# Kernel tuning notes

Hardware: AMD Instinct MI355X
Metric: run time of the kernel (lower is better)

The kernel has to match this reference:

```python
import jax, jax.numpy as jnp
import numpy as np

B, T, DQ, DV, A, F, K = 64, 1024, 1024, 512, 512, 32, 31


def setup_inputs() -> dict:
    key = jax.random.key(0)
    ks = jax.random.split(key, 8)
    query = jax.random.normal(ks[0], (B, DQ), jnp.float32)
    values = jax.random.normal(ks[1], (B, T, DV), jnp.float32)
    # decoder-step states (as produced by init_states)
    attention_cum = jnp.zeros((B, T), jnp.float32)
    attention_old = jnp.zeros((B, T), jnp.float32)
    alpha = jnp.concatenate([jnp.ones((B, 1), jnp.float32),
                             jnp.zeros((B, T - 1), jnp.float32) + 1e-7], axis=1)
    # learned parameters (Glorot-ish scaling)
    W_query = jax.random.normal(ks[2], (DQ, A), jnp.float32) / np.sqrt(DQ)
    W_inputs = jax.random.normal(ks[3], (DV, A), jnp.float32) / np.sqrt(DV)
    v_w = jax.random.normal(ks[4], (A, 1), jnp.float32) / np.sqrt(A)
    v_b = jnp.zeros((1,), jnp.float32)
    loc_kernel = jax.random.normal(ks[5], (K, 2, F), jnp.float32) / np.sqrt(K * 2)  # WIO
    W_loc = jax.random.normal(ks[6], (F, A), jnp.float32) / np.sqrt(F)
    return {"query": query, "values": values, "attention_cum": attention_cum,
            "attention_old": attention_old, "alpha": alpha,
            "W_query": W_query, "W_inputs": W_inputs, "v_w": v_w, "v_b": v_b,
            "loc_kernel": loc_kernel, "W_loc": W_loc}


def reference(query, values, attention_cum, attention_old, alpha,
              W_query, W_inputs, v_w, v_b, loc_kernel, W_loc):
    # process_values: cached projection of encoder memory  [B,T,A]
    processed_values = jnp.einsum('btd,da->bta', values, W_inputs)
    # location features: conv over stacked (old, cum) attention  [B,T,2]->[B,T,F]
    attn_cat = jnp.stack([attention_old, attention_cum], axis=2)
    conv = jax.lax.conv_general_dilated(attn_cat, loc_kernel, window_strides=(1,),
                                        padding='SAME',
                                        dimension_numbers=('NWC', 'WIO', 'NWC'))
    processed_attn = jnp.einsum('btf,fa->bta', conv, W_loc)
    # query projection  [B,1,A]
    processed_query = (query @ W_query)[:, None, :]
    # additive score  [B,T]
    score = (jnp.tanh(processed_values + processed_query + processed_attn) @ v_w)[..., 0] + v_b
    scores_norm = jax.nn.softmax(score, axis=-1)
    # forward attention recursion
    fwd_shifted = jnp.pad(alpha[:, :-1], ((0, 0), (1, 0)))
    new_alpha = (0.5 * alpha + 0.5 * fwd_shifted + 1e-8) * scores_norm
    new_alpha = new_alpha / jnp.sum(new_alpha, axis=1, keepdims=True)
    attn_weights = new_alpha
    # updated states
    new_cum = attention_cum + scores_norm
    new_old = attn_weights
    # context vector  [B,DV]
    context = jnp.einsum('bt,btd->bd', attn_weights, values)
    return (context, attn_weights, new_cum, new_old, new_alpha)
```

## Files before the change

kernel.cpp:

```cpp
#include <hip/hip_runtime.h>
#include <hip/hip_bf16.h>
#include <cstdint>
#include <cstddef>

#define B 64
#define T 1024
#define DQ 1024
#define DV 512
#define A_DIM 512
#define F_DIM 32
#define KW 31
#define M_TOT (B*T)
#define KEXT2 576
#define NCH 9

typedef __attribute__((ext_vector_type(8))) short short8;
typedef __attribute__((ext_vector_type(4))) short short4v;
typedef __attribute__((ext_vector_type(4))) float f32x4;

static __device__ __forceinline__ unsigned short f2bf(float f) {
    unsigned int u = __builtin_bit_cast(unsigned int, f);
    u += 0x7fffu + ((u >> 16) & 1u);
    return (unsigned short)(u >> 16);
}
static __device__ __forceinline__ float bf2f(unsigned short h) {
    return __builtin_bit_cast(float, (unsigned int)h << 16);
}
static __device__ __forceinline__ short8 pack8(float4 x0, float4 x1) {
    short8 pk;
    pk[0] = (short)f2bf(x0.x); pk[1] = (short)f2bf(x0.y);
    pk[2] = (short)f2bf(x0.z); pk[3] = (short)f2bf(x0.w);
    pk[4] = (short)f2bf(x1.x); pk[5] = (short)f2bf(x1.y);
    pk[6] = (short)f2bf(x1.z); pk[7] = (short)f2bf(x1.w);
    return pk;
}
static __device__ __forceinline__ float tanh_fast(float x) {
    float e = __expf(2.0f * x);
    return 1.0f - 2.0f * __builtin_amdgcn_rcpf(e + 1.0f);
}

#define LDSDMA16(gptr, lptr)                                                        \
    __builtin_amdgcn_global_load_lds(                                               \
        (const __attribute__((address_space(1))) void*)(const void*)(gptr),         \
        (__attribute__((address_space(3))) void*)(void*)(lptr), 16, 0, 0)

__global__ void prep_kernel(const float* __restrict__ values,
                            const float* __restrict__ query, const float* __restrict__ Wq,
                            const float* __restrict__ Wi, const float* __restrict__ Wl,
                            const float* __restrict__ old_, const float* __restrict__ cum_,
                            const float* __restrict__ lk,
                            unsigned short* __restrict__ vbf, float* __restrict__ pq,
                            float* __restrict__ score, unsigned short* __restrict__ Bt,
                            unsigned short* __restrict__ convb) {
    __shared__ __align__(16) char smem[16640];
    int bid = blockIdx.x, tid = threadIdx.x;
    if (bid < 4096) {
        size_t base = (size_t)bid * 8192 + (size_t)tid * 8;
        #pragma unroll
        for (int j = 0; j < 4; ++j) {
            size_t idx = base + (size_t)j * 2048;
            float4 x0 = *(const float4*)(values + idx);
            float4 x1 = *(const float4*)(values + idx + 4);
            *(short8*)(vbf + idx) = pack8(x0, x1);
        }
    } else if (bid < 4608) {
        float (*red)[64] = (float(*)[64])smem;
        int pid = bid - 4096;
        int gid = pid * 256 + tid;
        if (gid < M_TOT) score[gid] = 0.f;
        int b = pid >> 3, a0 = (pid & 7) * 64;
        int al = tid & 63, ks = tid >> 6;
        const float* qr = query + (size_t)b * DQ + ks * 256;
        const float* wc = Wq + (size_t)(ks * 256) * A_DIM + a0 + al;
        float acc = 0.f;
        #pragma unroll 8
        for (int k = 0; k < 256; ++k) acc += qr[k] * wc[(size_t)k * A_DIM];
        red[ks][al] = acc;
        __syncthreads();
        if (ks == 0)
            pq[b * A_DIM + a0 + al] = red[0][al] + red[1][al] + red[2][al] + red[3][al];
    } else if (bid < 4680) {
        float (*tile)[65] = (float(*)[65])smem;
        int tb = bid - 4608;
        if (tb < 64) {
            int k0 = (tb >> 3) * 64, a0 = (tb & 7) * 64;
            int al = tid & 63, ko = tid >> 6;
            #pragma unroll
            for (int j = 0; j < 16; ++j) {
                int kl = j * 4 + ko;
                tile[kl][al] = Wi[(size_t)(k0 + kl) * A_DIM + a0 + al];
            }
            __syncthreads();
            int kl2 = tid & 63, ao = tid >> 6;
            #pragma unroll
            for (int j = 0; j < 16; ++j) {
                int al2 = j * 4 + ao;
                Bt[(size_t)(a0 + al2) * KEXT2 + k0 + kl2] = f2bf(tile[kl2][al2]);
            }
        } else {
            int a0 = (tb - 64) * 64;
            int al = tid & 63, ko = tid >> 6;
            #pragma unroll
            for (int j = 0; j < 8; ++j) {
                int kl = j * 4 + ko;
                tile[kl][al] = Wl[(size_t)kl * A_DIM + a0 + al];
            }
            __syncthreads();
            int kl2 = tid & 31, ao = tid >> 5;
            #pragma unroll
            for (int j = 0; j < 8; ++j) {
                int al2 = j * 8 + ao;
                Bt[(size_t)(a0 + al2) * KEXT2 + DV + kl2] = f2bf(tile[kl2][al2]);
            }
            #pragma unroll
            for (int j = 0; j < 8; ++j) {
                int idx = j * 256 + tid;
                int a_l = idx >> 5, kp = idx & 31;
                Bt[(size_t)(a0 + a_l) * KEXT2 + 544 + kp] = 0;
            }
        }
    } else {
        float* sOld = (float*)smem;
        float* sCum = sOld + 94;
        float* sLK  = sCum + 94;
        int cid = bid - 4680;
        int b = cid >> 4, t0 = (cid & 15) * 64;
        int tl = tid & 63, fg = tid >> 6;
        for (int j = tid; j < 94; j += 256) {
            int tt = t0 - 15 + j;
            bool ok = (tt >= 0 && tt < T);
            sOld[j] = ok ? old_[b * T + tt] : 0.f;
            sCum[j] = ok ? cum_[b * T + tt] : 0.f;
        }
        for (int j = tid; j < KW * 2 * F_DIM; j += 256) sLK[j] = lk[j];
        __syncthreads();
        float acc[8];
        #pragma unroll
        for (int f = 0; f < 8; ++f) acc[f] = 0.f;
        for (int k = 0; k < KW; ++k) {
            float o = sOld[tl + k], c = sCum[tl + k];
            const float* lo = &sLK[(k * 2 + 0) * F_DIM + fg * 8];
            const float* lc = &sLK[(k * 2 + 1) * F_DIM + fg * 8];
            #pragma unroll
            for (int f = 0; f < 8; ++f) acc[f] += o * lo[f] + c * lc[f];
        }
        short8 pk;
        #pragma unroll
        for (int f = 0; f < 8; ++f) pk[f] = (short)f2bf(acc[f]);
        unsigned short* dst = convb + (size_t)(b * T + t0 + tl) * 64 + fg * 8;
        *(short8*)dst = pk;
        *(short8*)(dst + 32) = (short8)0;
    }
}

template<bool VBF>
__launch_bounds__(256, 3)
__global__ void gemm_score(const float* __restrict__ values,
                           const unsigned short* __restrict__ vbf,
                           const unsigned short* __restrict__ Bt,
                           const unsigned short* __restrict__ convb,
                           const float* __restrict__ pq,
                           const float* __restrict__ vw,
                           float* __restrict__ score) {
    __shared__ __align__(16) short sA[128 * 64];
    __shared__ __align__(16) short sB[128 * 64];
    __shared__ float sPQ[128];
    __shared__ float sVW[128];
    int tid = threadIdx.x;
    int x = blockIdx.x & 7, l = blockIdx.x >> 3;
    int mt = x * 64 + (l >> 2), nq = l & 3;
    int m0 = mt * 128, n0 = nq * 128;
    int b = m0 >> 10;
    if (tid < 128) { sPQ[tid] = pq[b * A_DIM + n0 + tid]; sVW[tid] = vw[n0 + tid]; }
    int w = tid >> 6, lane = tid & 63, q = lane >> 4, l15 = lane & 15;
    int wm = w & 1, wn = w >> 1;
    f32x4 acc[4][4];
    #pragma unroll
    for (int mi = 0; mi < 4; ++mi)
        #pragma unroll
        for (int ni = 0; ni < 4; ++ni) acc[mi][ni] = (f32x4)0.f;

    for (int c = 0; c < NCH; ++c) {
        __syncthreads();
        #pragma unroll
        for (int j = 0; j < 4; ++j) {
            int slot = j * 256 + tid;
            int row = slot >> 3, seg = ((slot & 7) - row) & 7;
            const unsigned short* gB = Bt + (size_t)(n0 + row) * KEXT2 + c * 64 + seg * 8;
            LDSDMA16(gB, &sB[(j * 256 + w * 64) * 8]);
        }
        if (VBF) {
            #pragma unroll
            for (int j = 0; j < 4; ++j) {
                int slot = j * 256 + tid;
                int row = slot >> 3, seg = ((slot & 7) - row) & 7;
                const unsigned short* gA = (c < 8)
                    ? vbf + (size_t)(m0 + row) * DV + c * 64 + seg * 8
                    : convb + (size_t)(m0 + row) * 64 + seg * 8;
                LDSDMA16(gA, &sA[(j * 256 + w * 64) * 8]);
            }
        } else {
            #pragma unroll
            for (int jj = 0; jj < 4; ++jj) {
                int slot = tid * 4 + jj;
                int row = slot >> 3, sl = slot & 7, seg = (sl - row) & 7;
                short8 pk;
                if (c < 8) {
                    const float* s0 = values + (size_t)(m0 + row) * DV + c * 64 + seg * 8;
                    pk = pack8(*(const float4*)s0, *(const float4*)(s0 + 4));
                } else {
                    pk = *(const short8*)(convb + (size_t)(m0 + row) * 64 + seg * 8);
                }
                *(short8*)&sA[slot * 8] = pk;
            }
        }
        __syncthreads();
        #pragma unroll
        for (int h = 0; h < 2; ++h) {
            short8 af[4], bfr[4];
            int sgl = h * 4 + q;
            #pragma unroll
            for (int mi = 0; mi < 4; ++mi) {
                int r = wm * 64 + mi * 16 + l15;
                af[mi] = *(const short8*)&sA[r * 64 + (((sgl + r) & 7) << 3)];
            }
            #pragma unroll
            for (int ni = 0; ni < 4; ++ni) {
                int r = wn * 64 + ni * 16 + l15;
                bfr[ni] = *(const short8*)&sB[r * 64 + (((sgl + r) & 7) << 3)];
            }
            #pragma unroll
            for (int mi = 0; mi < 4; ++mi)
                #pragma unroll
                for (int ni = 0; ni < 4; ++ni)
                    acc[mi][ni] = __builtin_amdgcn_mfma_f32_16x16x32_bf16(af[mi], bfr[ni], acc[mi][ni], 0, 0, 0);
        }
    }
    #pragma unroll
    for (int mi = 0; mi < 4; ++mi) {
        #pragma unroll
        for (int r = 0; r < 4; ++r) {
            float s = 0.f;
            #pragma unroll
            for (int ni = 0; ni < 4; ++ni) {
                int col = wn * 64 + ni * 16 + l15;
                float xv = acc[mi][ni][r] + sPQ[col];
                s += tanh_fast(xv) * sVW[col];
            }
            #pragma unroll
            for (int off = 1; off < 16; off <<= 1) s += __shfl_xor(s, off, 64);
            if (l15 == 0)
                atomicAdd(&score[m0 + wm * 64 + mi * 16 + q * 4 + r], s);
        }
    }
}

__global__ void softmax_fwd(const float* __restrict__ score,
                            const float* __restrict__ alpha,
                            const float* __restrict__ cum,
                            float* __restrict__ out) {
    int b = blockIdx.x, t = threadIdx.x;
    __shared__ float sred[16];
    __shared__ float sbc;
    float sc = score[b * T + t];
    int wid = t >> 6, lane = t & 63;
    float m = sc;
    #pragma unroll
    for (int off = 32; off; off >>= 1) m = fmaxf(m, __shfl_xor(m, off, 64));
    if (lane == 0) sred[wid] = m;
    __syncthreads();
    if (t == 0) { float mm = sred[0]; for (int i = 1; i < 16; ++i) mm = fmaxf(mm, sred[i]); sbc = mm; }
    __syncthreads();
    float M = sbc;
    float e = __expf(sc - M);
    float s = e;
    #pragma unroll
    for (int off = 32; off; off >>= 1) s += __shfl_xor(s, off, 64);
    __syncthreads();
    if (lane == 0) sred[wid] = s;
    __syncthreads();
    if (t == 0) { float ss = 0.f; for (int i = 0; i < 16; ++i) ss += sred[i]; sbc = ss; }
    __syncthreads();
    float sn = e / sbc;
    float a_t = alpha[b * T + t];
    float a_p = (t > 0) ? alpha[b * T + t - 1] : 0.f;
    float ua = (0.5f * (a_t + a_p) + 1e-8f) * sn;
    float u = ua;
    #pragma unroll
    for (int off = 32; off; off >>= 1) u += __shfl_xor(u, off, 64);
    __syncthreads();
    if (lane == 0) sred[wid] = u;
    __syncthreads();
    if (t == 0) { float ss = 0.f; for (int i = 0; i < 16; ++i) ss += sred[i]; sbc = ss; }
    __syncthreads();
    float wgt = ua / sbc;
    float* attnw  = out + B * DV;
    float* ncum   = attnw + B * T;
    float* nold   = ncum + B * T;
    float* nalpha = nold + B * T;
    attnw[b * T + t]  = wgt;
    ncum[b * T + t]   = cum[b * T + t] + sn;
    nold[b * T + t]   = wgt;
    nalpha[b * T + t] = wgt;
    if (t < DV) out[b * DV + t] = 0.f;
}

__global__ void context_kernel(const float* __restrict__ values,
                               const unsigned short* __restrict__ vbf,
                               int use_bf, float* __restrict__ out) {
    __shared__ float red[4][256];
    const float* attnw = out + B * DV;
    int b = blockIdx.x >> 3, tq = (blockIdx.x >> 1) & 3, dh = blockIdx.x & 1;
    int sub = threadIdx.x >> 6, dg = threadIdx.x & 63;
    int t0 = tq * 256 + sub * 64;
    int d0 = dh * 256 + dg * 4;
    float acc[4];
    #pragma unroll
    for (int f = 0; f < 4; ++f) acc[f] = 0.f;
    if (use_bf) {
        for (int tt = 0; tt < 64; ++tt) {
            int t = t0 + tt;
            float wgt = attnw[b * T + t];
            short4v v = *(const short4v*)(vbf + (size_t)(b * T + t) * DV + d0);
            #pragma unroll
            for (int f = 0; f < 4; ++f) acc[f] += wgt * bf2f((unsigned short)v[f]);
        }
    } else {
        for (int tt = 0; tt < 64; ++tt) {
            int t = t0 + tt;
            float wgt = attnw[b * T + t];
            float4 xv = *(const float4*)(values + (size_t)(b * T + t) * DV + d0);
            acc[0] += wgt * xv.x; acc[1] += wgt * xv.y;
            acc[2] += wgt * xv.z; acc[3] += wgt * xv.w;
        }
    }
    #pragma unroll
    for (int f = 0; f < 4; ++f) red[sub][dg * 4 + f] = acc[f];
    __syncthreads();
    if (sub == 0) {
        #pragma unroll
        for (int f = 0; f < 4; ++f) {
            int di = dg * 4 + f;
            float s = red[0][di] + red[1][di] + red[2][di] + red[3][di];
            atomicAdd(&out[b * DV + dh * 256 + di], s);
        }
    }
}

extern "C" void kernel_launch(void* const* d_in, const int* in_sizes, int n_in,
                              void* d_out, int out_size, void* d_ws, size_t ws_size,
                              hipStream_t stream) {
    const float* query  = (const float*)d_in[0];
    const float* values = (const float*)d_in[1];
    const float* cum    = (const float*)d_in[2];
    const float* old_   = (const float*)d_in[3];
    const float* alpha  = (const float*)d_in[4];
    const float* Wq     = (const float*)d_in[5];
    const float* Wi     = (const float*)d_in[6];
    const float* vw     = (const float*)d_in[7];
    const float* lk     = (const float*)d_in[9];
    const float* Wl     = (const float*)d_in[10];
    float* out = (float*)d_out;
    char* ws = (char*)d_ws;
    float* ws_pq            = (float*)(ws);
    float* ws_score         = (float*)(ws + 131072);
    unsigned short* ws_Bt   = (unsigned short*)(ws + 393216);
    unsigned short* ws_conv = (unsigned short*)(ws + 1048576);
    unsigned short* ws_vbf  = (unsigned short*)(ws + 16777216);
    const bool big = ws_size >= (size_t)88080384;

    if (big) {
        prep_kernel<<<5704, 256, 0, stream>>>(values, query, Wq, Wi, Wl, old_, cum, lk,
                                              ws_vbf, ws_pq, ws_score, ws_Bt, ws_conv);
        gemm_score<true><<<2048, 256, 0, stream>>>(values, ws_vbf, ws_Bt, ws_conv, ws_pq, vw, ws_score);
    } else {
        prep_kernel<<<1608, 256, 0, stream>>>(values, query, Wq, Wi, Wl, old_, cum, lk,
                                              ws_vbf, ws_pq, ws_score, ws_Bt, ws_conv);
        gemm_score<false><<<2048, 256, 0, stream>>>(values, ws_vbf, ws_Bt, ws_conv, ws_pq, vw, ws_score);
    }
    softmax_fwd<<<64, 1024, 0, stream>>>(ws_score, alpha, cum, out);
    context_kernel<<<512, 256, 0, stream>>>(values, ws_vbf, big ? 1 : 0, out);
}
```

Baseline: 305.4 us.

## Drop bf16 pre-conversion pass; convert values to bf16 inside GEMM tile loads

Removes the prep pass that converts all of values to a bf16 workspace copy. The GEMM now loads fp32 values directly, packs them to bf16 into LDS with all loads issued before any stores, and uses LDS DMA only for the conv feature chunk. The context kernel reads fp32 values instead of the bf16 copy. This avoids a full extra read and write of the large values tensor, but the GEMM and context kernels now read twice as many bytes for values, and the conversion work moves into the GEMM main loop.

```diff
diff --git a/kernel.cpp b/kernel.cpp
--- a/kernel.cpp
+++ b/kernel.cpp
@@ -15,16 +15,12 @@
 #define NCH 9
 
 typedef __attribute__((ext_vector_type(8))) short short8;
-typedef __attribute__((ext_vector_type(4))) short short4v;
 typedef __attribute__((ext_vector_type(4))) float f32x4;
 
 static __device__ __forceinline__ unsigned short f2bf(float f) {
     unsigned int u = __builtin_bit_cast(unsigned int, f);
     u += 0x7fffu + ((u >> 16) & 1u);
     return (unsigned short)(u >> 16);
-}
-static __device__ __forceinline__ float bf2f(unsigned short h) {
-    return __builtin_bit_cast(float, (unsigned int)h << 16);
 }
 static __device__ __forceinline__ short8 pack8(float4 x0, float4 x1) {
     short8 pk;
@@ -44,28 +40,18 @@
         (const __attribute__((address_space(1))) void*)(const void*)(gptr),         \
         (__attribute__((address_space(3))) void*)(void*)(lptr), 16, 0, 0)
 
-__global__ void prep_kernel(const float* __restrict__ values,
-                            const float* __restrict__ query, const float* __restrict__ Wq,
+__global__ void prep_kernel(const float* __restrict__ query, const float* __restrict__ Wq,
                             const float* __restrict__ Wi, const float* __restrict__ Wl,
                             const float* __restrict__ old_, const float* __restrict__ cum_,
                             const float* __restrict__ lk,
-                            unsigned short* __restrict__ vbf, float* __restrict__ pq,
+                            float* __restrict__ pq,
                             float* __restrict__ score, unsigned short* __restrict__ Bt,
                             unsigned short* __restrict__ convb) {
     __shared__ __align__(16) char smem[16640];
     int bid = blockIdx.x, tid = threadIdx.x;
-    if (bid < 4096) {
-        size_t base = (size_t)bid * 8192 + (size_t)tid * 8;
-        #pragma unroll
-        for (int j = 0; j < 4; ++j) {
-            size_t idx = base + (size_t)j * 2048;
-            float4 x0 = *(const float4*)(values + idx);
-            float4 x1 = *(const float4*)(values + idx + 4);
-            *(short8*)(vbf + idx) = pack8(x0, x1);
-        }
-    } else if (bid < 4608) {
+    if (bid < 512) {
         float (*red)[64] = (float(*)[64])smem;
-        int pid = bid - 4096;
+        int pid = bid;
         int gid = pid * 256 + tid;
         if (gid < M_TOT) score[gid] = 0.f;
         int b = pid >> 3, a0 = (pid & 7) * 64;
@@ -79,9 +65,9 @@
         __syncthreads();
         if (ks == 0)
             pq[b * A_DIM + a0 + al] = red[0][al] + red[1][al] + red[2][al] + red[3][al];
-    } else if (bid < 4680) {
+    } else if (bid < 584) {
         float (*tile)[65] = (float(*)[65])smem;
-        int tb = bid - 4608;
+        int tb = bid - 512;
         if (tb < 64) {
             int k0 = (tb >> 3) * 64, a0 = (tb & 7) * 64;
             int al = tid & 63, ko = tid >> 6;
@@ -123,7 +109,7 @@
         float* sOld = (float*)smem;
         float* sCum = sOld + 94;
         float* sLK  = sCum + 94;
-        int cid = bid - 4680;
+        int cid = bid - 584;
         int b = cid >> 4, t0 = (cid & 15) * 64;
         int tl = tid & 63, fg = tid >> 6;
         for (int j = tid; j < 94; j += 256) {
@@ -153,10 +139,8 @@
     }
 }
 
-template<bool VBF>
 __launch_bounds__(256, 3)
 __global__ void gemm_score(const float* __restrict__ values,
-                           const unsigned short* __restrict__ vbf,
                            const unsigned short* __restrict__ Bt,
                            const unsigned short* __restrict__ convb,
                            const float* __restrict__ pq,
@@ -174,6 +158,15 @@
     if (tid < 128) { sPQ[tid] = pq[b * A_DIM + n0 + tid]; sVW[tid] = vw[n0 + tid]; }
     int w = tid >> 6, lane = tid & 63, q = lane >> 4, l15 = lane & 15;
     int wm = w & 1, wn = w >> 1;
+    const float* aSrc[4];
+    int aSlot[4];
+    #pragma unroll
+    for (int jj = 0; jj < 4; ++jj) {
+        int slot = tid * 4 + jj;
+        int row = slot >> 3, sl = slot & 7, seg = (sl - row) & 7;
+        aSrc[jj] = values + (size_t)(m0 + row) * DV + seg * 8;
+        aSlot[jj] = slot;
+    }
     f32x4 acc[4][4];
     #pragma unroll
     for (int mi = 0; mi < 4; ++mi)
@@ -189,29 +182,24 @@
             const unsigned short* gB = Bt + (size_t)(n0 + row) * KEXT2 + c * 64 + seg * 8;
             LDSDMA16(gB, &sB[(j * 256 + w * 64) * 8]);
         }
-        if (VBF) {
+        if (c < 8) {
+            float4 x0[4], x1[4];
+            #pragma unroll
+            for (int jj = 0; jj < 4; ++jj) {
+                const float* s0 = aSrc[jj] + c * 64;
+                x0[jj] = *(const float4*)s0;
+                x1[jj] = *(const float4*)(s0 + 4);
+            }
+            #pragma unroll
+            for (int jj = 0; jj < 4; ++jj)
+                *(short8*)&sA[aSlot[jj] * 8] = pack8(x0[jj], x1[jj]);
+        } else {
             #pragma unroll
             for (int j = 0; j < 4; ++j) {
                 int slot = j * 256 + tid;
                 int row = slot >> 3, seg = ((slot & 7) - row) & 7;
-                const unsigned short* gA = (c < 8)
-                    ? vbf + (size_t)(m0 + row) * DV + c * 64 + seg * 8
-                    : convb + (size_t)(m0 + row) * 64 + seg * 8;
-                LDSDMA16(gA, &sA[(j * 256 + w * 64) * 8]);
-            }
-        } else {
-            #pragma unroll
-            for (int jj = 0; jj < 4; ++jj) {
-                int slot = tid * 4 + jj;
-                int row = slot >> 3, sl = slot & 7, seg = (sl - row) & 7;
-                short8 pk;
-                if (c < 8) {
-                    const float* s0 = values + (size_t)(m0 + row) * DV + c * 64 + seg * 8;
-                    pk = pack8(*(const float4*)s0, *(const float4*)(s0 + 4));
-                } else {
-                    pk = *(const short8*)(convb + (size_t)(m0 + row) * 64 + seg * 8);
-                }
-                *(short8*)&sA[slot * 8] = pk;
+                LDSDMA16(convb + (size_t)(m0 + row) * 64 + seg * 8,
+                         &sA[(j * 256 + w * 64) * 8]);
             }
         }
         __syncthreads();
@@ -306,8 +294,7 @@
 }
 
 __global__ void context_kernel(const float* __restrict__ values,
-                               const unsigned short* __restrict__ vbf,
-                               int use_bf, float* __restrict__ out) {
+                               float* __restrict__ out) {
     __shared__ float red[4][256];
     const float* attnw = out + B * DV;
     int b = blockIdx.x >> 3, tq = (blockIdx.x >> 1) & 3, dh = blockIdx.x & 1;
@@ -317,22 +304,12 @@
     float acc[4];
     #pragma unroll
     for (int f = 0; f < 4; ++f) acc[f] = 0.f;
-    if (use_bf) {
-        for (int tt = 0; tt < 64; ++tt) {
-            int t = t0 + tt;
-            float wgt = attnw[b * T + t];
-            short4v v = *(const short4v*)(vbf + (size_t)(b * T + t) * DV + d0);
-            #pragma unroll
-            for (int f = 0; f < 4; ++f) acc[f] += wgt * bf2f((unsigned short)v[f]);
-        }
-    } else {
-        for (int tt = 0; tt < 64; ++tt) {
-            int t = t0 + tt;
-            float wgt = attnw[b * T + t];
-            float4 xv = *(const float4*)(values + (size_t)(b * T + t) * DV + d0);
-            acc[0] += wgt * xv.x; acc[1] += wgt * xv.y;
-            acc[2] += wgt * xv.z; acc[3] += wgt * xv.w;
-        }
+    for (int tt = 0; tt < 64; ++tt) {
+        int t = t0 + tt;
+        float wgt = attnw[b * T + t];
+        float4 xv = *(const float4*)(values + (size_t)(b * T + t) * DV + d0);
+        acc[0] += wgt * xv.x; acc[1] += wgt * xv.y;
+        acc[2] += wgt * xv.z; acc[3] += wgt * xv.w;
     }
     #pragma unroll
     for (int f = 0; f < 4; ++f) red[sub][dg * 4 + f] = acc[f];
@@ -366,18 +343,10 @@
     float* ws_score         = (float*)(ws + 131072);
     unsigned short* ws_Bt   = (unsigned short*)(ws + 393216);
     unsigned short* ws_conv = (unsigned short*)(ws + 1048576);
-    unsigned short* ws_vbf  = (unsigned short*)(ws + 16777216);
-    const bool big = ws_size >= (size_t)88080384;
-
-    if (big) {
-        prep_kernel<<<5704, 256, 0, stream>>>(values, query, Wq, Wi, Wl, old_, cum, lk,
-                                              ws_vbf, ws_pq, ws_score, ws_Bt, ws_conv);
-        gemm_score<true><<<2048, 256, 0, stream>>>(values, ws_vbf, ws_Bt, ws_conv, ws_pq, vw, ws_score);
-    } else {
-        prep_kernel<<<1608, 256, 0, stream>>>(values, query, Wq, Wi, Wl, old_, cum, lk,
-                                              ws_vbf, ws_pq, ws_score, ws_Bt, ws_conv);
-        gemm_score<false><<<2048, 256, 0, stream>>>(values, ws_vbf, ws_Bt, ws_conv, ws_pq, vw, ws_score);
-    }
+
+    prep_kernel<<<1608, 256, 0, stream>>>(query, Wq, Wi, Wl, old_, cum, lk,
+                                          ws_pq, ws_score, ws_Bt, ws_conv);
+    gemm_score<<<2048, 256, 0, stream>>>(values, ws_Bt, ws_conv, ws_pq, vw, ws_score);
     softmax_fwd<<<64, 1024, 0, stream>>>(ws_score, alpha, cum, out);
-    context_kernel<<<512, 256, 0, stream>>>(values, ws_vbf, big ? 1 : 0, out);
-}
+    context_kernel<<<512, 256, 0, stream>>>(values, out);
+}
```

Result: slower. 324.3 us (+6.2%).
